# Performance work log

Measured on AMD Instinct MI355X. Metric: run time of the kernel, lower is better.

The kernel has to match this reference:

```python
import jax, jax.numpy as jnp
import numpy as np

EMBED_DIM = 256
NUM_HEADS = 8
PROJ_DIM = EMBED_DIM // NUM_HEADS


def setup_inputs() -> dict:
    key = jax.random.key(0)
    ks = jax.random.split(key, 5)
    scale = 1.0 / np.sqrt(EMBED_DIM)
    inputs = jax.random.normal(ks[0], (2, 12, 12, 12, EMBED_DIM), dtype=jnp.float32)
    Wq = jax.random.normal(ks[1], (EMBED_DIM, EMBED_DIM), dtype=jnp.float32) * scale
    Wk = jax.random.normal(ks[2], (EMBED_DIM, EMBED_DIM), dtype=jnp.float32) * scale
    Wv = jax.random.normal(ks[3], (EMBED_DIM, EMBED_DIM), dtype=jnp.float32) * scale
    Wo = jax.random.normal(ks[4], (EMBED_DIM, EMBED_DIM), dtype=jnp.float32) * scale
    z = jnp.zeros((EMBED_DIM,), dtype=jnp.float32)
    return {"inputs": inputs, "Wq": Wq, "bq": z, "Wk": Wk, "bk": z,
            "Wv": Wv, "bv": z, "Wo": Wo, "bo": z}


def reference(inputs, Wq, bq, Wk, bk, Wv, bv, Wo, bo):
    B, h, w, d, E = inputs.shape
    S = h * w * d  # flattened spatial sequence
    x = inputs.reshape(B, S, E)
    # projections + head split: [B, S, E] -> [B, H, S, P]
    def split_heads(t):
        return t.reshape(B, S, NUM_HEADS, PROJ_DIM).transpose(0, 2, 1, 3)
    q = split_heads(x @ Wq + bq)
    k = split_heads(x @ Wk + bk)
    v = split_heads(x @ Wv + bv)
    # NOTE: original module does NOT scale by 1/sqrt(proj_dim)
    scores = jnp.einsum('bhsp,bhtp->bhst', q, k)  # [B, H, S, S]
    attn = jax.nn.softmax(scores, axis=-1)
    out = jnp.einsum('bhst,bhtp->bhsp', attn, v)  # [B, H, S, P]
    out = out.transpose(0, 2, 1, 3).reshape(B, h, w, d, E)
    return out @ Wo + bo
```

## Files before the change

### kernel.cpp

```cpp
#include <hip/hip_runtime.h>
#include <math.h>

#define EMBED 256
#define HEADS 8
#define PDIM  32
#define BATCH 2
#define SEQ   1728
#define NTOK  (BATCH*SEQ)
#define NE    (NTOK*EMBED)
#define NKT   (SEQ/64)
#define LOG2E 1.44269504088896f

typedef __attribute__((ext_vector_type(8))) __bf16 bf16x8;
typedef __attribute__((ext_vector_type(4))) float  f32x4;
typedef unsigned short ushort_t;
typedef unsigned int   uint_t;

static __device__ __forceinline__ unsigned short f2bf_rne(float f) {
    union { float f; unsigned u; } x; x.f = f;
    unsigned r = x.u + 0x7fffu + ((x.u >> 16) & 1u);
    return (unsigned short)(r >> 16);
}
union v8cast { uint4 u; bf16x8 v; };

static __device__ __forceinline__ void cvt8_hilo(const float f[8], bf16x8& hi, bf16x8& lo) {
    uint4 ph, pl;
    uint_t* phv = (uint_t*)&ph; uint_t* plv = (uint_t*)&pl;
    #pragma unroll
    for (int j = 0; j < 4; ++j) {
        const float f0 = f[2 * j], f1 = f[2 * j + 1];
        const uint_t u0 = __float_as_uint(f0) + 0x8000u;
        const uint_t u1 = __float_as_uint(f1) + 0x8000u;
        phv[j] = __builtin_amdgcn_perm(u1, u0, 0x07060302u);
        const float l0 = f0 - __uint_as_float(u0 & 0xFFFF0000u);
        const float l1 = f1 - __uint_as_float(u1 & 0xFFFF0000u);
        plv[j] = __builtin_amdgcn_perm(__float_as_uint(l1) + 0x8000u,
                                       __float_as_uint(l0) + 0x8000u, 0x07060302u);
    }
    v8cast ch; ch.u = ph; hi = ch.v;
    v8cast cl; cl.u = pl; lo = cl.v;
}

__global__ __launch_bounds__(64) void qkv_gemm_kernel(
    const float* __restrict__ x,
    const float* __restrict__ Wq, const float* __restrict__ bq,
    const float* __restrict__ Wk, const float* __restrict__ bk,
    const float* __restrict__ Wv, const float* __restrict__ bv,
    ushort_t* __restrict__ qo, ushort_t* __restrict__ ko, ushort_t* __restrict__ vt)
{
    const int lane = threadIdx.x, li = lane & 15, quad = lane >> 4;
    const int m0 = blockIdx.x * 64, n0 = blockIdx.y * 32, z = blockIdx.z;
    const float* __restrict__ W    = (z == 0) ? Wq : (z == 1) ? Wk : Wv;
    const float* __restrict__ bias = (z == 0) ? bq : (z == 1) ? bk : bv;

    const float* ap = x + (size_t)(m0 + li) * EMBED + quad * 8;

    f32x4 acc[4][2];
    #pragma unroll
    for (int mt = 0; mt < 4; ++mt)
        #pragma unroll
        for (int nt = 0; nt < 2; ++nt)
            acc[mt][nt] = (f32x4){0.f, 0.f, 0.f, 0.f};

    #pragma unroll 2
    for (int k0 = 0; k0 < EMBED; k0 += 32) {
        bf16x8 ah[4], al[4];
        #pragma unroll
        for (int mt = 0; mt < 4; ++mt) {
            float af[8];
            *(float4*)&af[0] = *(const float4*)(ap + (size_t)mt * 16 * EMBED + k0);
            *(float4*)&af[4] = *(const float4*)(ap + (size_t)mt * 16 * EMBED + k0 + 4);
            cvt8_hilo(af, ah[mt], al[mt]);
        }
        bf16x8 bh[2], bl[2];
        #pragma unroll
        for (int nt = 0; nt < 2; ++nt) {
            const int n = n0 + nt * 16 + li;
            const float* wp = W + (size_t)(k0 + quad * 8) * EMBED + n;
            float bf[8];
            #pragma unroll
            for (int jj = 0; jj < 8; ++jj) bf[jj] = wp[(size_t)jj * EMBED];
            cvt8_hilo(bf, bh[nt], bl[nt]);
        }
        #pragma unroll
        for (int mt = 0; mt < 4; ++mt)
            #pragma unroll
            for (int nt = 0; nt < 2; ++nt) {
                acc[mt][nt] = __builtin_amdgcn_mfma_f32_16x16x32_bf16(ah[mt], bh[nt], acc[mt][nt], 0, 0, 0);
                acc[mt][nt] = __builtin_amdgcn_mfma_f32_16x16x32_bf16(al[mt], bh[nt], acc[mt][nt], 0, 0, 0);
                acc[mt][nt] = __builtin_amdgcn_mfma_f32_16x16x32_bf16(ah[mt], bl[nt], acc[mt][nt], 0, 0, 0);
            }
    }

    const int b = m0 / SEQ;
    const int sbase = m0 - b * SEQ;

    if (z <= 1) {
        ushort_t* __restrict__ dst = z ? ko : qo;
        #pragma unroll
        for (int nt = 0; nt < 2; ++nt) {
            const int gcol = n0 + nt * 16 + li;
            const int h = gcol >> 5, p = gcol & 31;
            const float bb = bias[gcol];
            ushort_t* base = dst + ((size_t)(b * HEADS + h) * SEQ) * PDIM + p;
            #pragma unroll
            for (int mt = 0; mt < 4; ++mt)
                #pragma unroll
                for (int r = 0; r < 4; ++r) {
                    const int s = sbase + mt * 16 + quad * 4 + r;
                    base[(size_t)s * PDIM] = f2bf_rne(acc[mt][nt][r] + bb);
                }
        }
    } else {
        #pragma unroll
        for (int nt = 0; nt < 2; ++nt) {
            const int gcol = n0 + nt * 16 + li;
            const int h = gcol >> 5, p = gcol & 31;
            const float bb = bias[gcol];
            ushort_t* base = vt + ((size_t)(b * HEADS + h) * PDIM + p) * SEQ;
            #pragma unroll
            for (int mt = 0; mt < 4; ++mt) {
                const int s0 = sbase + mt * 16 + quad * 4;
                ushort4 w;
                w.x = f2bf_rne(acc[mt][nt][0] + bb);
                w.y = f2bf_rne(acc[mt][nt][1] + bb);
                w.z = f2bf_rne(acc[mt][nt][2] + bb);
                w.w = f2bf_rne(acc[mt][nt][3] + bb);
                *(ushort4*)&base[s0] = w;
            }
        }
    }
}

__global__ __launch_bounds__(256) void attn_kernel(
    const ushort_t* __restrict__ q, const ushort_t* __restrict__ k,
    const ushort_t* __restrict__ vt, ushort_t* __restrict__ aob)
{
    const int t    = threadIdx.x;
    const int lane = t & 63;
    const int w    = t >> 6;
    const int li   = lane & 15;
    const int quad = lane >> 4;
    const int bh = blockIdx.y;
    const int b  = bh >> 3, h = bh & 7;
    const int q0 = blockIdx.x * 64 + w * 16;

    const ushort_t* __restrict__ qb = q  + (size_t)bh * SEQ * PDIM;
    const ushort_t* __restrict__ kb = k  + (size_t)bh * SEQ * PDIM;
    const ushort_t* __restrict__ vb = vt + (size_t)bh * PDIM * SEQ;

    __shared__ ushort_t Ks[2][64][40];
    __shared__ ushort_t Vs[2][32][72];
    __shared__ ushort_t Ps[4][16][72];

    const bf16x8 qfrag = *(const bf16x8*)(qb + (size_t)(q0 + li) * PDIM + quad * 8);

    const int jk = w * 16 + (lane >> 2), ck = (lane & 3) * 8;
    const int pv = w * 8 + (lane >> 3),  cv = (lane & 7) * 8;
    const ushort_t* kgp = kb + (size_t)jk * PDIM + ck;
    const ushort_t* vgp = vb + (size_t)pv * SEQ + cv;

    f32x4 o0 = {0.f, 0.f, 0.f, 0.f};
    f32x4 o1 = {0.f, 0.f, 0.f, 0.f};
    float m_run = -__builtin_inff(), l_run = 0.f;

    uint4 kreg = *(const uint4*)(kgp);
    uint4 vreg = *(const uint4*)(vgp);

    for (int kt = 0; kt < NKT; ++kt) {
        const int p = kt & 1;
        *(uint4*)&Ks[p][jk][ck] = kreg;
        *(uint4*)&Vs[p][pv][cv] = vreg;
        __syncthreads();
        if (kt + 1 < NKT) {
            kreg = *(const uint4*)(kgp + (size_t)(kt + 1) * 64 * PDIM);
            vreg = *(const uint4*)(vgp + (kt + 1) * 64);
        }

        const f32x4 zero = {0.f, 0.f, 0.f, 0.f};
        f32x4 st[4];
        #pragma unroll
        for (int jt = 0; jt < 4; ++jt) {
            const bf16x8 kf = *(const bf16x8*)&Ks[p][jt * 16 + li][quad * 8];
            st[jt] = __builtin_amdgcn_mfma_f32_16x16x32_bf16(kf, qfrag, zero, 0, 0, 0);
        }

        float tm = st[0][0];
        #pragma unroll
        for (int jt = 0; jt < 4; ++jt)
            #pragma unroll
            for (int r = 0; r < 4; ++r) tm = fmaxf(tm, st[jt][r]);
        tm = fmaxf(tm, __shfl_xor(tm, 16));
        tm = fmaxf(tm, __shfl_xor(tm, 32));
        const float mnew  = fmaxf(m_run, tm);
        const float negml = -(mnew * LOG2E);

        float ps = 0.f;
        #pragma unroll
        for (int jt = 0; jt < 4; ++jt) {
            const float p0 = __builtin_amdgcn_exp2f(fmaf(st[jt][0], LOG2E, negml));
            const float p1 = __builtin_amdgcn_exp2f(fmaf(st[jt][1], LOG2E, negml));
            const float p2 = __builtin_amdgcn_exp2f(fmaf(st[jt][2], LOG2E, negml));
            const float p3 = __builtin_amdgcn_exp2f(fmaf(st[jt][3], LOG2E, negml));
            ps += (p0 + p1) + (p2 + p3);
            uint2 pw;
            pw.x = __builtin_amdgcn_perm(__float_as_uint(p1) + 0x8000u,
                                         __float_as_uint(p0) + 0x8000u, 0x07060302u);
            pw.y = __builtin_amdgcn_perm(__float_as_uint(p3) + 0x8000u,
                                         __float_as_uint(p2) + 0x8000u, 0x07060302u);
            *(uint2*)&Ps[w][li][16 * jt + 4 * quad] = pw;
        }
        ps += __shfl_xor(ps, 16);
        ps += __shfl_xor(ps, 32);

        const float alpha = __builtin_amdgcn_exp2f(fmaf(m_run, LOG2E, negml));
        l_run = fmaf(l_run, alpha, ps);
        m_run = mnew;

        float af[4];
        #pragma unroll
        for (int r = 0; r < 4; ++r) af[r] = __shfl(alpha, 4 * quad + r);
        #pragma unroll
        for (int r = 0; r < 4; ++r) { o0[r] *= af[r]; o1[r] *= af[r]; }

        const bf16x8 pa0 = *(const bf16x8*)&Ps[w][li][8 * quad];
        const bf16x8 pa1 = *(const bf16x8*)&Ps[w][li][32 + 8 * quad];
        const bf16x8 vf00 = *(const bf16x8*)&Vs[p][li][quad * 8];
        const bf16x8 vf01 = *(const bf16x8*)&Vs[p][16 + li][quad * 8];
        const bf16x8 vf10 = *(const bf16x8*)&Vs[p][li][32 + quad * 8];
        const bf16x8 vf11 = *(const bf16x8*)&Vs[p][16 + li][32 + quad * 8];
        o0 = __builtin_amdgcn_mfma_f32_16x16x32_bf16(pa0, vf00, o0, 0, 0, 0);
        o0 = __builtin_amdgcn_mfma_f32_16x16x32_bf16(pa1, vf10, o0, 0, 0, 0);
        o1 = __builtin_amdgcn_mfma_f32_16x16x32_bf16(pa0, vf01, o1, 0, 0, 0);
        o1 = __builtin_amdgcn_mfma_f32_16x16x32_bf16(pa1, vf11, o1, 0, 0, 0);
    }

    float linv[4];
    #pragma unroll
    for (int r = 0; r < 4; ++r) linv[r] = 1.0f / __shfl(l_run, 4 * quad + r);
    #pragma unroll
    for (int r = 0; r < 4; ++r) {
        const int s = q0 + 4 * quad + r;
        ushort_t* row = aob + ((size_t)(b * SEQ + s)) * EMBED + h * PDIM;
        row[li]      = f2bf_rne(o0[r] * linv[r]);
        row[16 + li] = f2bf_rne(o1[r] * linv[r]);
    }
}

__global__ __launch_bounds__(64) void out_gemm_kernel(
    const ushort_t* __restrict__ a, const float* __restrict__ Wo,
    const float* __restrict__ bo, float* __restrict__ out)
{
    const int lane = threadIdx.x, li = lane & 15, quad = lane >> 4;
    const int m0 = blockIdx.x * 64, n0 = blockIdx.y * 16;

    const ushort_t* aph = a + (size_t)(m0 + li) * EMBED + quad * 8;

    f32x4 acc[4];
    #pragma unroll
    for (int mt = 0; mt < 4; ++mt) acc[mt] = (f32x4){0.f, 0.f, 0.f, 0.f};

    #pragma unroll 2
    for (int k0 = 0; k0 < EMBED; k0 += 32) {
        bf16x8 ah[4];
        #pragma unroll
        for (int mt = 0; mt < 4; ++mt)
            ah[mt] = *(const bf16x8*)(aph + (size_t)mt * 16 * EMBED + k0);
        const float* wp = Wo + (size_t)(k0 + quad * 8) * EMBED + n0 + li;
        uint4 pb;
        uint_t* pbv = (uint_t*)&pb;
        #pragma unroll
        for (int j = 0; j < 4; ++j) {
            const uint_t u0 = __float_as_uint(wp[(size_t)(2 * j) * EMBED])     + 0x8000u;
            const uint_t u1 = __float_as_uint(wp[(size_t)(2 * j + 1) * EMBED]) + 0x8000u;
            pbv[j] = __builtin_amdgcn_perm(u1, u0, 0x07060302u);
        }
        v8cast cb; cb.u = pb;
        #pragma unroll
        for (int mt = 0; mt < 4; ++mt)
            acc[mt] = __builtin_amdgcn_mfma_f32_16x16x32_bf16(ah[mt], cb.v, acc[mt], 0, 0, 0);
    }

    const float bb = bo[n0 + li];
    #pragma unroll
    for (int mt = 0; mt < 4; ++mt)
        #pragma unroll
        for (int r = 0; r < 4; ++r) {
            const int row = m0 + mt * 16 + quad * 4 + r;
            out[(size_t)row * EMBED + n0 + li] = acc[mt][r] + bb;
        }
}

extern "C" void kernel_launch(void* const* d_in, const int* in_sizes, int n_in,
                              void* d_out, int out_size, void* d_ws, size_t ws_size,
                              hipStream_t stream)
{
    const float* x  = (const float*)d_in[0];
    const float* Wq = (const float*)d_in[1];
    const float* bq = (const float*)d_in[2];
    const float* Wk = (const float*)d_in[3];
    const float* bk = (const float*)d_in[4];
    const float* Wv = (const float*)d_in[5];
    const float* bv = (const float*)d_in[6];
    const float* Wo = (const float*)d_in[7];
    const float* bo = (const float*)d_in[8];
    float* out = (float*)d_out;

    ushort_t* ws  = (ushort_t*)d_ws;
    ushort_t* qb  = ws;
    ushort_t* kb  = qb + (size_t)NE;
    ushort_t* vt  = kb + (size_t)NE;
    ushort_t* aob = vt + (size_t)NE;

    qkv_gemm_kernel<<<dim3(NTOK / 64, 8, 3), 64, 0, stream>>>(
        x, Wq, bq, Wk, bk, Wv, bv, qb, kb, vt);
    attn_kernel<<<dim3(SEQ / 64, BATCH * HEADS), 256, 0, stream>>>(qb, kb, vt, aob);
    out_gemm_kernel<<<dim3(NTOK / 64, 16), 64, 0, stream>>>(aob, Wo, bo, out);
}
```

Before: 121.5 us.

## Fuse QKV, attention and out-projection into one cooperative persistent kernel

Replaces three separate launches with one cooperative kernel of 432 blocks that runs the QKV GEMM tiles, then a grid sync, then attention, then another grid sync, then the output projection. The goal is to remove per-launch overhead and the idle tails between dependent stages. The output projection also uses smaller 32-row tiles so its work spreads over the persistent blocks. In exchange it pays for two grid-wide barriers, is limited to a fixed grid with 2 blocks per CU, and falls back to the old three-kernel path if the cooperative launch is not possible.

```diff
diff --git a/kernel.cpp b/kernel.cpp
--- a/kernel.cpp
+++ b/kernel.cpp
@@ -1,4 +1,5 @@
 #include <hip/hip_runtime.h>
+#include <hip/hip_cooperative_groups.h>
 #include <math.h>
 
 #define EMBED 256
@@ -10,6 +11,8 @@
 #define NE    (NTOK*EMBED)
 #define NKT   (SEQ/64)
 #define LOG2E 1.44269504088896f
+#define NBLK  432
+#define NTHR  256
 
 typedef __attribute__((ext_vector_type(8))) __bf16 bf16x8;
 typedef __attribute__((ext_vector_type(4))) float  f32x4;
@@ -41,6 +44,278 @@
     v8cast cl; cl.u = pl; lo = cl.v;
 }
 
+
+static __device__ __forceinline__ void qkv_tile(
+    int wg, int li, int quad,
+    const float* __restrict__ x,
+    const float* __restrict__ Wq, const float* __restrict__ bq,
+    const float* __restrict__ Wk, const float* __restrict__ bk,
+    const float* __restrict__ Wv, const float* __restrict__ bv,
+    ushort_t* __restrict__ qg, ushort_t* __restrict__ kg, ushort_t* __restrict__ vg)
+{
+    const int z   = wg / 432;
+    const int rem = wg - z * 432;
+    const int my  = rem % 54, ny = rem / 54;
+    const int m0  = my * 64, n0 = ny * 32;
+    const float* __restrict__ W    = (z == 0) ? Wq : (z == 1) ? Wk : Wv;
+    const float* __restrict__ bias = (z == 0) ? bq : (z == 1) ? bk : bv;
+
+    const float* ap = x + (size_t)(m0 + li) * EMBED + quad * 8;
+
+    f32x4 acc[4][2];
+    #pragma unroll
+    for (int mt = 0; mt < 4; ++mt)
+        #pragma unroll
+        for (int nt = 0; nt < 2; ++nt)
+            acc[mt][nt] = (f32x4){0.f, 0.f, 0.f, 0.f};
+
+    #pragma unroll 2
+    for (int k0 = 0; k0 < EMBED; k0 += 32) {
+        bf16x8 ah[4], al[4];
+        #pragma unroll
+        for (int mt = 0; mt < 4; ++mt) {
+            float af[8];
+            *(float4*)&af[0] = *(const float4*)(ap + (size_t)mt * 16 * EMBED + k0);
+            *(float4*)&af[4] = *(const float4*)(ap + (size_t)mt * 16 * EMBED + k0 + 4);
+            cvt8_hilo(af, ah[mt], al[mt]);
+        }
+        bf16x8 bh[2], bl[2];
+        #pragma unroll
+        for (int nt = 0; nt < 2; ++nt) {
+            const int n = n0 + nt * 16 + li;
+            const float* wp = W + (size_t)(k0 + quad * 8) * EMBED + n;
+            float bf[8];
+            #pragma unroll
+            for (int jj = 0; jj < 8; ++jj) bf[jj] = wp[(size_t)jj * EMBED];
+            cvt8_hilo(bf, bh[nt], bl[nt]);
+        }
+        #pragma unroll
+        for (int mt = 0; mt < 4; ++mt)
+            #pragma unroll
+            for (int nt = 0; nt < 2; ++nt) {
+                acc[mt][nt] = __builtin_amdgcn_mfma_f32_16x16x32_bf16(ah[mt], bh[nt], acc[mt][nt], 0, 0, 0);
+                acc[mt][nt] = __builtin_amdgcn_mfma_f32_16x16x32_bf16(al[mt], bh[nt], acc[mt][nt], 0, 0, 0);
+                acc[mt][nt] = __builtin_amdgcn_mfma_f32_16x16x32_bf16(ah[mt], bl[nt], acc[mt][nt], 0, 0, 0);
+            }
+    }
+
+    const int b = m0 / SEQ;
+    const int sbase = m0 - b * SEQ;
+
+    if (z <= 1) {
+        ushort_t* __restrict__ dst = z ? kg : qg;
+        #pragma unroll
+        for (int nt = 0; nt < 2; ++nt) {
+            const int gcol = n0 + nt * 16 + li;
+            const int h = gcol >> 5, p = gcol & 31;
+            const float bb = bias[gcol];
+            ushort_t* base = dst + ((size_t)(b * HEADS + h) * SEQ) * PDIM + p;
+            #pragma unroll
+            for (int mt = 0; mt < 4; ++mt)
+                #pragma unroll
+                for (int r = 0; r < 4; ++r) {
+                    const int s = sbase + mt * 16 + quad * 4 + r;
+                    base[(size_t)s * PDIM] = f2bf_rne(acc[mt][nt][r] + bb);
+                }
+        }
+    } else {
+        #pragma unroll
+        for (int nt = 0; nt < 2; ++nt) {
+            const int gcol = n0 + nt * 16 + li;
+            const int h = gcol >> 5, p = gcol & 31;
+            const float bb = bias[gcol];
+            ushort_t* base = vg + ((size_t)(b * HEADS + h) * PDIM + p) * SEQ;
+            #pragma unroll
+            for (int mt = 0; mt < 4; ++mt) {
+                const int s0 = sbase + mt * 16 + quad * 4;
+                ushort4 wv4;
+                wv4.x = f2bf_rne(acc[mt][nt][0] + bb);
+                wv4.y = f2bf_rne(acc[mt][nt][1] + bb);
+                wv4.z = f2bf_rne(acc[mt][nt][2] + bb);
+                wv4.w = f2bf_rne(acc[mt][nt][3] + bb);
+                *(ushort4*)&base[s0] = wv4;
+            }
+        }
+    }
+}
+
+static __device__ __forceinline__ void outproj_tile(
+    int wg, int li, int quad,
+    const ushort_t* __restrict__ ag, const float* __restrict__ Wo,
+    const float* __restrict__ bo, float* __restrict__ out)
+{
+    const int my = wg % 108, ny = wg / 108;
+    const int m0 = my * 32, n0 = ny * 16;
+
+    const ushort_t* aph = ag + (size_t)(m0 + li) * EMBED + quad * 8;
+
+    f32x4 acc[2];
+    acc[0] = (f32x4){0.f, 0.f, 0.f, 0.f};
+    acc[1] = (f32x4){0.f, 0.f, 0.f, 0.f};
+
+    #pragma unroll 2
+    for (int k0 = 0; k0 < EMBED; k0 += 32) {
+        const bf16x8 a0 = *(const bf16x8*)(aph + k0);
+        const bf16x8 a1 = *(const bf16x8*)(aph + 16 * EMBED + k0);
+        const float* wp = Wo + (size_t)(k0 + quad * 8) * EMBED + n0 + li;
+        uint4 pb;
+        uint_t* pbv = (uint_t*)&pb;
+        #pragma unroll
+        for (int j = 0; j < 4; ++j) {
+            const uint_t u0 = __float_as_uint(wp[(size_t)(2 * j) * EMBED])     + 0x8000u;
+            const uint_t u1 = __float_as_uint(wp[(size_t)(2 * j + 1) * EMBED]) + 0x8000u;
+            pbv[j] = __builtin_amdgcn_perm(u1, u0, 0x07060302u);
+        }
+        v8cast cb; cb.u = pb;
+        acc[0] = __builtin_amdgcn_mfma_f32_16x16x32_bf16(a0, cb.v, acc[0], 0, 0, 0);
+        acc[1] = __builtin_amdgcn_mfma_f32_16x16x32_bf16(a1, cb.v, acc[1], 0, 0, 0);
+    }
+
+    const float bb = bo[n0 + li];
+    #pragma unroll
+    for (int mt = 0; mt < 2; ++mt)
+        #pragma unroll
+        for (int r = 0; r < 4; ++r) {
+            const int row = m0 + mt * 16 + quad * 4 + r;
+            out[(size_t)row * EMBED + n0 + li] = acc[mt][r] + bb;
+        }
+}
+
+__global__ __launch_bounds__(256, 2) void fused_mhsa_kernel(
+    const float* __restrict__ x,
+    const float* __restrict__ Wq, const float* __restrict__ bq,
+    const float* __restrict__ Wk, const float* __restrict__ bk,
+    const float* __restrict__ Wv, const float* __restrict__ bv,
+    const float* __restrict__ Wo, const float* __restrict__ bo,
+    float* __restrict__ out,
+    ushort_t* __restrict__ qg, ushort_t* __restrict__ kg,
+    ushort_t* __restrict__ vg, ushort_t* __restrict__ ag)
+{
+    const int t    = threadIdx.x;
+    const int lane = t & 63, w = t >> 6;
+    const int li   = lane & 15, quad = lane >> 4;
+    const int bid  = blockIdx.x;
+
+    {
+        const int wg = bid * 4 + w;
+        if (wg < 1296)
+            qkv_tile(wg, li, quad, x, Wq, bq, Wk, bk, Wv, bv, qg, kg, vg);
+    }
+
+    cooperative_groups::this_grid().sync();
+
+    {
+        const int bh = bid & 15, qt = bid >> 4;
+        const int b  = bh >> 3, h = bh & 7;
+        const int q0 = qt * 64 + w * 16;
+
+        const ushort_t* __restrict__ qb = qg + (size_t)bh * SEQ * PDIM;
+        const ushort_t* __restrict__ kb = kg + (size_t)bh * SEQ * PDIM;
+        const ushort_t* __restrict__ vb = vg + (size_t)bh * PDIM * SEQ;
+
+        __shared__ ushort_t Ks[2][64][40];
+        __shared__ ushort_t Vs[2][32][72];
+        __shared__ ushort_t Ps[4][16][72];
+
+        const bf16x8 qfrag = *(const bf16x8*)(qb + (size_t)(q0 + li) * PDIM + quad * 8);
+
+        const int jk = w * 16 + (lane >> 2), ck = (lane & 3) * 8;
+        const int pv = w * 8 + (lane >> 3),  cv = (lane & 7) * 8;
+        const ushort_t* kgp = kb + (size_t)jk * PDIM + ck;
+        const ushort_t* vgp = vb + (size_t)pv * SEQ + cv;
+
+        f32x4 o0 = {0.f, 0.f, 0.f, 0.f};
+        f32x4 o1 = {0.f, 0.f, 0.f, 0.f};
+        float m_run = -__builtin_inff(), l_run = 0.f;
+
+        uint4 kreg = *(const uint4*)(kgp);
+        uint4 vreg = *(const uint4*)(vgp);
+
+        for (int kt = 0; kt < NKT; ++kt) {
+            const int p = kt & 1;
+            *(uint4*)&Ks[p][jk][ck] = kreg;
+            *(uint4*)&Vs[p][pv][cv] = vreg;
+            __syncthreads();
+            if (kt + 1 < NKT) {
+                kreg = *(const uint4*)(kgp + (size_t)(kt + 1) * 64 * PDIM);
+                vreg = *(const uint4*)(vgp + (kt + 1) * 64);
+            }
+
+            const f32x4 zero = {0.f, 0.f, 0.f, 0.f};
+            f32x4 st[4];
+            #pragma unroll
+            for (int jt = 0; jt < 4; ++jt) {
+                const bf16x8 kf = *(const bf16x8*)&Ks[p][jt * 16 + li][quad * 8];
+                st[jt] = __builtin_amdgcn_mfma_f32_16x16x32_bf16(kf, qfrag, zero, 0, 0, 0);
+            }
+
+            float tm = st[0][0];
+            #pragma unroll
+            for (int jt = 0; jt < 4; ++jt)
+                #pragma unroll
+                for (int r = 0; r < 4; ++r) tm = fmaxf(tm, st[jt][r]);
+            tm = fmaxf(tm, __shfl_xor(tm, 16));
+            tm = fmaxf(tm, __shfl_xor(tm, 32));
+            const float mnew  = fmaxf(m_run, tm);
+            const float negml = -(mnew * LOG2E);
+
+            float ps = 0.f;
+            #pragma unroll
+            for (int jt = 0; jt < 4; ++jt) {
+                const float p0 = __builtin_amdgcn_exp2f(fmaf(st[jt][0], LOG2E, negml));
+                const float p1 = __builtin_amdgcn_exp2f(fmaf(st[jt][1], LOG2E, negml));
+                const float p2 = __builtin_amdgcn_exp2f(fmaf(st[jt][2], LOG2E, negml));
+                const float p3 = __builtin_amdgcn_exp2f(fmaf(st[jt][3], LOG2E, negml));
+                ps += (p0 + p1) + (p2 + p3);
+                uint2 pw;
+                pw.x = __builtin_amdgcn_perm(__float_as_uint(p1) + 0x8000u,
+                                             __float_as_uint(p0) + 0x8000u, 0x07060302u);
+                pw.y = __builtin_amdgcn_perm(__float_as_uint(p3) + 0x8000u,
+                                             __float_as_uint(p2) + 0x8000u, 0x07060302u);
+                *(uint2*)&Ps[w][li][16 * jt + 4 * quad] = pw;
+            }
+            ps += __shfl_xor(ps, 16);
+            ps += __shfl_xor(ps, 32);
+
+            const float alpha = __builtin_amdgcn_exp2f(fmaf(m_run, LOG2E, negml));
+            l_run = fmaf(l_run, alpha, ps);
+            m_run = mnew;
+
+            float af[4];
+            #pragma unroll
+            for (int r = 0; r < 4; ++r) af[r] = __shfl(alpha, 4 * quad + r);
+            #pragma unroll
+            for (int r = 0; r < 4; ++r) { o0[r] *= af[r]; o1[r] *= af[r]; }
+
+            const bf16x8 pa0 = *(const bf16x8*)&Ps[w][li][8 * quad];
+            const bf16x8 pa1 = *(const bf16x8*)&Ps[w][li][32 + 8 * quad];
+            const bf16x8 vf00 = *(const bf16x8*)&Vs[p][li][quad * 8];
+            const bf16x8 vf01 = *(const bf16x8*)&Vs[p][16 + li][quad * 8];
+            const bf16x8 vf10 = *(const bf16x8*)&Vs[p][li][32 + quad * 8];
+            const bf16x8 vf11 = *(const bf16x8*)&Vs[p][16 + li][32 + quad * 8];
+            o0 = __builtin_amdgcn_mfma_f32_16x16x32_bf16(pa0, vf00, o0, 0, 0, 0);
+            o0 = __builtin_amdgcn_mfma_f32_16x16x32_bf16(pa1, vf10, o0, 0, 0, 0);
+            o1 = __builtin_amdgcn_mfma_f32_16x16x32_bf16(pa0, vf01, o1, 0, 0, 0);
+            o1 = __builtin_amdgcn_mfma_f32_16x16x32_bf16(pa1, vf11, o1, 0, 0, 0);
+        }
+
+        float linv[4];
+        #pragma unroll
+        for (int r = 0; r < 4; ++r) linv[r] = 1.0f / __shfl(l_run, 4 * quad + r);
+        #pragma unroll
+        for (int r = 0; r < 4; ++r) {
+            const int s = q0 + 4 * quad + r;
+            ushort_t* row = ag + ((size_t)(b * SEQ + s)) * EMBED + h * PDIM;
+            row[li]      = f2bf_rne(o0[r] * linv[r]);
+            row[16 + li] = f2bf_rne(o1[r] * linv[r]);
+        }
+    }
+
+    cooperative_groups::this_grid().sync();
+
+    outproj_tile(bid * 4 + w, li, quad, ag, Wo, bo, out);
+}
+
 __global__ __launch_bounds__(64) void qkv_gemm_kernel(
     const float* __restrict__ x,
     const float* __restrict__ Wq, const float* __restrict__ bq,
@@ -49,87 +324,10 @@
     ushort_t* __restrict__ qo, ushort_t* __restrict__ ko, ushort_t* __restrict__ vt)
 {
     const int lane = threadIdx.x, li = lane & 15, quad = lane >> 4;
-    const int m0 = blockIdx.x * 64, n0 = blockIdx.y * 32, z = blockIdx.z;
-    const float* __restrict__ W    = (z == 0) ? Wq : (z == 1) ? Wk : Wv;
-    const float* __restrict__ bias = (z == 0) ? bq : (z == 1) ? bk : bv;
-
-    const float* ap = x + (size_t)(m0 + li) * EMBED + quad * 8;
-
-    f32x4 acc[4][2];
-    #pragma unroll
-    for (int mt = 0; mt < 4; ++mt)
-        #pragma unroll
-        for (int nt = 0; nt < 2; ++nt)
-            acc[mt][nt] = (f32x4){0.f, 0.f, 0.f, 0.f};
-
-    #pragma unroll 2
-    for (int k0 = 0; k0 < EMBED; k0 += 32) {
-        bf16x8 ah[4], al[4];
-        #pragma unroll
-        for (int mt = 0; mt < 4; ++mt) {
-            float af[8];
-            *(float4*)&af[0] = *(const float4*)(ap + (size_t)mt * 16 * EMBED + k0);
-            *(float4*)&af[4] = *(const float4*)(ap + (size_t)mt * 16 * EMBED + k0 + 4);
-            cvt8_hilo(af, ah[mt], al[mt]);
-        }
-        bf16x8 bh[2], bl[2];
-        #pragma unroll
-        for (int nt = 0; nt < 2; ++nt) {
-            const int n = n0 + nt * 16 + li;
-            const float* wp = W + (size_t)(k0 + quad * 8) * EMBED + n;
-            float bf[8];
-            #pragma unroll
-            for (int jj = 0; jj < 8; ++jj) bf[jj] = wp[(size_t)jj * EMBED];
-            cvt8_hilo(bf, bh[nt], bl[nt]);
-        }
-        #pragma unroll
-        for (int mt = 0; mt < 4; ++mt)
-            #pragma unroll
-            for (int nt = 0; nt < 2; ++nt) {
-                acc[mt][nt] = __builtin_amdgcn_mfma_f32_16x16x32_bf16(ah[mt], bh[nt], acc[mt][nt], 0, 0, 0);
-                acc[mt][nt] = __builtin_amdgcn_mfma_f32_16x16x32_bf16(al[mt], bh[nt], acc[mt][nt], 0, 0, 0);
-                acc[mt][nt] = __builtin_amdgcn_mfma_f32_16x16x32_bf16(ah[mt], bl[nt], acc[mt][nt], 0, 0, 0);
-            }
-    }
-
-    const int b = m0 / SEQ;
-    const int sbase = m0 - b * SEQ;
-
-    if (z <= 1) {
-        ushort_t* __restrict__ dst = z ? ko : qo;
-        #pragma unroll
-        for (int nt = 0; nt < 2; ++nt) {
-            const int gcol = n0 + nt * 16 + li;
-            const int h = gcol >> 5, p = gcol & 31;
-            const float bb = bias[gcol];
-            ushort_t* base = dst + ((size_t)(b * HEADS + h) * SEQ) * PDIM + p;
-            #pragma unroll
-            for (int mt = 0; mt < 4; ++mt)
-                #pragma unroll
-                for (int r = 0; r < 4; ++r) {
-                    const int s = sbase + mt * 16 + quad * 4 + r;
-                    base[(size_t)s * PDIM] = f2bf_rne(acc[mt][nt][r] + bb);
-                }
-        }
-    } else {
-        #pragma unroll
-        for (int nt = 0; nt < 2; ++nt) {
-            const int gcol = n0 + nt * 16 + li;
-            const int h = gcol >> 5, p = gcol & 31;
-            const float bb = bias[gcol];
-            ushort_t* base = vt + ((size_t)(b * HEADS + h) * PDIM + p) * SEQ;
-            #pragma unroll
-            for (int mt = 0; mt < 4; ++mt) {
-                const int s0 = sbase + mt * 16 + quad * 4;
-                ushort4 w;
-                w.x = f2bf_rne(acc[mt][nt][0] + bb);
-                w.y = f2bf_rne(acc[mt][nt][1] + bb);
-                w.z = f2bf_rne(acc[mt][nt][2] + bb);
-                w.w = f2bf_rne(acc[mt][nt][3] + bb);
-                *(ushort4*)&base[s0] = w;
-            }
-        }
-    }
+    const int wg = (blockIdx.z * 8 + blockIdx.y) * 54 + blockIdx.x;
+    qkv_tile(blockIdx.z * 432 + blockIdx.y * 54 + blockIdx.x, li, quad,
+             x, Wq, bq, Wk, bk, Wv, bv, qo, ko, vt);
+    (void)wg;
 }
 
 __global__ __launch_bounds__(256) void attn_kernel(
@@ -137,10 +335,8 @@
     const ushort_t* __restrict__ vt, ushort_t* __restrict__ aob)
 {
     const int t    = threadIdx.x;
-    const int lane = t & 63;
-    const int w    = t >> 6;
-    const int li   = lane & 15;
-    const int quad = lane >> 4;
+    const int lane = t & 63, w = t >> 6;
+    const int li   = lane & 15, quad = lane >> 4;
     const int bh = blockIdx.y;
     const int b  = bh >> 3, h = bh & 7;
     const int q0 = blockIdx.x * 64 + w * 16;
@@ -252,43 +448,7 @@
     const float* __restrict__ bo, float* __restrict__ out)
 {
     const int lane = threadIdx.x, li = lane & 15, quad = lane >> 4;
-    const int m0 = blockIdx.x * 64, n0 = blockIdx.y * 16;
-
-    const ushort_t* aph = a + (size_t)(m0 + li) * EMBED + quad * 8;
-
-    f32x4 acc[4];
-    #pragma unroll
-    for (int mt = 0; mt < 4; ++mt) acc[mt] = (f32x4){0.f, 0.f, 0.f, 0.f};
-
-    #pragma unroll 2
-    for (int k0 = 0; k0 < EMBED; k0 += 32) {
-        bf16x8 ah[4];
-        #pragma unroll
-        for (int mt = 0; mt < 4; ++mt)
-            ah[mt] = *(const bf16x8*)(aph + (size_t)mt * 16 * EMBED + k0);
-        const float* wp = Wo + (size_t)(k0 + quad * 8) * EMBED + n0 + li;
-        uint4 pb;
-        uint_t* pbv = (uint_t*)&pb;
-        #pragma unroll
-        for (int j = 0; j < 4; ++j) {
-            const uint_t u0 = __float_as_uint(wp[(size_t)(2 * j) * EMBED])     + 0x8000u;
-            const uint_t u1 = __float_as_uint(wp[(size_t)(2 * j + 1) * EMBED]) + 0x8000u;
-            pbv[j] = __builtin_amdgcn_perm(u1, u0, 0x07060302u);
-        }
-        v8cast cb; cb.u = pb;
-        #pragma unroll
-        for (int mt = 0; mt < 4; ++mt)
-            acc[mt] = __builtin_amdgcn_mfma_f32_16x16x32_bf16(ah[mt], cb.v, acc[mt], 0, 0, 0);
-    }
-
-    const float bb = bo[n0 + li];
-    #pragma unroll
-    for (int mt = 0; mt < 4; ++mt)
-        #pragma unroll
-        for (int r = 0; r < 4; ++r) {
-            const int row = m0 + mt * 16 + quad * 4 + r;
-            out[(size_t)row * EMBED + n0 + li] = acc[mt][r] + bb;
-        }
+    outproj_tile(blockIdx.y * 108 + blockIdx.x, li, quad, a, Wo, bo, out);
 }
 
 extern "C" void kernel_launch(void* const* d_in, const int* in_sizes, int n_in,
@@ -306,14 +466,28 @@
     const float* bo = (const float*)d_in[8];
     float* out = (float*)d_out;
 
-    ushort_t* ws  = (ushort_t*)d_ws;
-    ushort_t* qb  = ws;
-    ushort_t* kb  = qb + (size_t)NE;
-    ushort_t* vt  = kb + (size_t)NE;
-    ushort_t* aob = vt + (size_t)NE;
-
-    qkv_gemm_kernel<<<dim3(NTOK / 64, 8, 3), 64, 0, stream>>>(
-        x, Wq, bq, Wk, bk, Wv, bv, qb, kb, vt);
-    attn_kernel<<<dim3(SEQ / 64, BATCH * HEADS), 256, 0, stream>>>(qb, kb, vt, aob);
-    out_gemm_kernel<<<dim3(NTOK / 64, 16), 64, 0, stream>>>(aob, Wo, bo, out);
-}
+    ushort_t* ws = (ushort_t*)d_ws;
+    ushort_t* qg = ws;
+    ushort_t* kg = qg + (size_t)NE;
+    ushort_t* vg = kg + (size_t)NE;
+    ushort_t* ag = vg + (size_t)NE;
+
+    int maxb = 0;
+    hipError_t qerr = hipOccupancyMaxActiveBlocksPerMultiprocessor(
+        &maxb, (const void*)fused_mhsa_kernel, NTHR, 0);
+    bool coop_done = false;
+    if (qerr == hipSuccess && maxb >= 2) {
+        void* args[] = { (void*)&x, (void*)&Wq, (void*)&bq, (void*)&Wk, (void*)&bk,
+                         (void*)&Wv, (void*)&bv, (void*)&Wo, (void*)&bo, (void*)&out,
+                         (void*)&qg, (void*)&kg, (void*)&vg, (void*)&ag };
+        hipError_t lerr = hipLaunchCooperativeKernel((const void*)fused_mhsa_kernel,
+                                                     dim3(NBLK), dim3(NTHR), args, 0, stream);
+        coop_done = (lerr == hipSuccess);
+    }
+    if (!coop_done) {
+        qkv_gemm_kernel<<<dim3(54, 8, 3), 64, 0, stream>>>(
+            x, Wq, bq, Wk, bk, Wv, bv, qg, kg, vg);
+        attn_kernel<<<dim3(SEQ / 64, BATCH * HEADS), 256, 0, stream>>>(qg, kg, vg, ag);
+        out_gemm_kernel<<<dim3(108, 16), 64, 0, stream>>>(ag, Wo, bo, out);
+    }
+}
```

Result: slower. 237.5 us (+95.5%).

## Split attention KV range across wave pairs and merge partial softmax results

Applied to the files above, without the earlier changes.

The attention kernel now handles 32 queries per block instead of 64. Each pair of waves splits the 27 key tiles into two halves (tiles 0–13 and 13–26, with the second half skipping its first tile). Partial outputs and running max/sum are combined through shared memory at the end. This doubles the grid to 864 blocks to improve occupancy and latency hiding across CUs. The cost is a shared-memory merge step and extra synchronisation, and each thread loads two vectors per tile.

```diff
diff --git a/kernel.cpp b/kernel.cpp
--- a/kernel.cpp
+++ b/kernel.cpp
@@ -8,7 +8,6 @@
 #define SEQ   1728
 #define NTOK  (BATCH*SEQ)
 #define NE    (NTOK*EMBED)
-#define NKT   (SEQ/64)
 #define LOG2E 1.44269504088896f
 
 typedef __attribute__((ext_vector_type(8))) __bf16 bf16x8;
@@ -121,12 +120,12 @@
             #pragma unroll
             for (int mt = 0; mt < 4; ++mt) {
                 const int s0 = sbase + mt * 16 + quad * 4;
-                ushort4 w;
-                w.x = f2bf_rne(acc[mt][nt][0] + bb);
-                w.y = f2bf_rne(acc[mt][nt][1] + bb);
-                w.z = f2bf_rne(acc[mt][nt][2] + bb);
-                w.w = f2bf_rne(acc[mt][nt][3] + bb);
-                *(ushort4*)&base[s0] = w;
+                ushort4 wv4;
+                wv4.x = f2bf_rne(acc[mt][nt][0] + bb);
+                wv4.y = f2bf_rne(acc[mt][nt][1] + bb);
+                wv4.z = f2bf_rne(acc[mt][nt][2] + bb);
+                wv4.w = f2bf_rne(acc[mt][nt][3] + bb);
+                *(ushort4*)&base[s0] = wv4;
             }
         }
     }
@@ -137,13 +136,13 @@
     const ushort_t* __restrict__ vt, ushort_t* __restrict__ aob)
 {
     const int t    = threadIdx.x;
-    const int lane = t & 63;
-    const int w    = t >> 6;
-    const int li   = lane & 15;
-    const int quad = lane >> 4;
+    const int lane = t & 63, w = t >> 6;
+    const int li   = lane & 15, quad = lane >> 4;
+    const int pr   = w >> 1;
+    const int c    = w & 1;
     const int bh = blockIdx.y;
     const int b  = bh >> 3, h = bh & 7;
-    const int q0 = blockIdx.x * 64 + w * 16;
+    const int q0 = blockIdx.x * 32 + pr * 16;
 
     const ushort_t* __restrict__ qb = q  + (size_t)bh * SEQ * PDIM;
     const ushort_t* __restrict__ kb = k  + (size_t)bh * SEQ * PDIM;
@@ -152,11 +151,13 @@
     __shared__ ushort_t Ks[2][64][40];
     __shared__ ushort_t Vs[2][32][72];
     __shared__ ushort_t Ps[4][16][72];
+    __shared__ float OS[2][16][32];
+    __shared__ float mS[2][16], lS[2][16];
 
     const bf16x8 qfrag = *(const bf16x8*)(qb + (size_t)(q0 + li) * PDIM + quad * 8);
 
-    const int jk = w * 16 + (lane >> 2), ck = (lane & 3) * 8;
-    const int pv = w * 8 + (lane >> 3),  cv = (lane & 7) * 8;
+    const int jk = pr * 32 + (lane >> 1), ck = (lane & 1) * 8;
+    const int pv = pr * 16 + (lane >> 2), cv = (lane & 3) * 8;
     const ushort_t* kgp = kb + (size_t)jk * PDIM + ck;
     const ushort_t* vgp = vb + (size_t)pv * SEQ + cv;
 
@@ -164,86 +165,117 @@
     f32x4 o1 = {0.f, 0.f, 0.f, 0.f};
     float m_run = -__builtin_inff(), l_run = 0.f;
 
-    uint4 kreg = *(const uint4*)(kgp);
-    uint4 vreg = *(const uint4*)(vgp);
-
-    for (int kt = 0; kt < NKT; ++kt) {
-        const int p = kt & 1;
-        *(uint4*)&Ks[p][jk][ck] = kreg;
-        *(uint4*)&Vs[p][pv][cv] = vreg;
+    const int kt0 = c ? 13 : 0;
+
+    uint4 kr0 = *(const uint4*)(kgp + (size_t)kt0 * 64 * PDIM);
+    uint4 kr1 = *(const uint4*)(kgp + (size_t)kt0 * 64 * PDIM + 16);
+    uint4 vr0 = *(const uint4*)(vgp + kt0 * 64);
+    uint4 vr1 = *(const uint4*)(vgp + kt0 * 64 + 32);
+
+    for (int it = 0; it < 14; ++it) {
         __syncthreads();
-        if (kt + 1 < NKT) {
-            kreg = *(const uint4*)(kgp + (size_t)(kt + 1) * 64 * PDIM);
-            vreg = *(const uint4*)(vgp + (kt + 1) * 64);
-        }
-
-        const f32x4 zero = {0.f, 0.f, 0.f, 0.f};
-        f32x4 st[4];
-        #pragma unroll
-        for (int jt = 0; jt < 4; ++jt) {
-            const bf16x8 kf = *(const bf16x8*)&Ks[p][jt * 16 + li][quad * 8];
-            st[jt] = __builtin_amdgcn_mfma_f32_16x16x32_bf16(kf, qfrag, zero, 0, 0, 0);
-        }
-
-        float tm = st[0][0];
-        #pragma unroll
-        for (int jt = 0; jt < 4; ++jt)
-            #pragma unroll
-            for (int r = 0; r < 4; ++r) tm = fmaxf(tm, st[jt][r]);
-        tm = fmaxf(tm, __shfl_xor(tm, 16));
-        tm = fmaxf(tm, __shfl_xor(tm, 32));
-        const float mnew  = fmaxf(m_run, tm);
-        const float negml = -(mnew * LOG2E);
-
-        float ps = 0.f;
-        #pragma unroll
-        for (int jt = 0; jt < 4; ++jt) {
-            const float p0 = __builtin_amdgcn_exp2f(fmaf(st[jt][0], LOG2E, negml));
-            const float p1 = __builtin_amdgcn_exp2f(fmaf(st[jt][1], LOG2E, negml));
-            const float p2 = __builtin_amdgcn_exp2f(fmaf(st[jt][2], LOG2E, negml));
-            const float p3 = __builtin_amdgcn_exp2f(fmaf(st[jt][3], LOG2E, negml));
-            ps += (p0 + p1) + (p2 + p3);
-            uint2 pw;
-            pw.x = __builtin_amdgcn_perm(__float_as_uint(p1) + 0x8000u,
-                                         __float_as_uint(p0) + 0x8000u, 0x07060302u);
-            pw.y = __builtin_amdgcn_perm(__float_as_uint(p3) + 0x8000u,
-                                         __float_as_uint(p2) + 0x8000u, 0x07060302u);
-            *(uint2*)&Ps[w][li][16 * jt + 4 * quad] = pw;
-        }
-        ps += __shfl_xor(ps, 16);
-        ps += __shfl_xor(ps, 32);
-
-        const float alpha = __builtin_amdgcn_exp2f(fmaf(m_run, LOG2E, negml));
-        l_run = fmaf(l_run, alpha, ps);
-        m_run = mnew;
-
-        float af[4];
-        #pragma unroll
-        for (int r = 0; r < 4; ++r) af[r] = __shfl(alpha, 4 * quad + r);
-        #pragma unroll
-        for (int r = 0; r < 4; ++r) { o0[r] *= af[r]; o1[r] *= af[r]; }
-
-        const bf16x8 pa0 = *(const bf16x8*)&Ps[w][li][8 * quad];
-        const bf16x8 pa1 = *(const bf16x8*)&Ps[w][li][32 + 8 * quad];
-        const bf16x8 vf00 = *(const bf16x8*)&Vs[p][li][quad * 8];
-        const bf16x8 vf01 = *(const bf16x8*)&Vs[p][16 + li][quad * 8];
-        const bf16x8 vf10 = *(const bf16x8*)&Vs[p][li][32 + quad * 8];
-        const bf16x8 vf11 = *(const bf16x8*)&Vs[p][16 + li][32 + quad * 8];
-        o0 = __builtin_amdgcn_mfma_f32_16x16x32_bf16(pa0, vf00, o0, 0, 0, 0);
-        o0 = __builtin_amdgcn_mfma_f32_16x16x32_bf16(pa1, vf10, o0, 0, 0, 0);
-        o1 = __builtin_amdgcn_mfma_f32_16x16x32_bf16(pa0, vf01, o1, 0, 0, 0);
-        o1 = __builtin_amdgcn_mfma_f32_16x16x32_bf16(pa1, vf11, o1, 0, 0, 0);
-    }
-
-    float linv[4];
-    #pragma unroll
-    for (int r = 0; r < 4; ++r) linv[r] = 1.0f / __shfl(l_run, 4 * quad + r);
-    #pragma unroll
-    for (int r = 0; r < 4; ++r) {
-        const int s = q0 + 4 * quad + r;
-        ushort_t* row = aob + ((size_t)(b * SEQ + s)) * EMBED + h * PDIM;
-        row[li]      = f2bf_rne(o0[r] * linv[r]);
-        row[16 + li] = f2bf_rne(o1[r] * linv[r]);
+        *(uint4*)&Ks[c][jk][ck]      = kr0;
+        *(uint4*)&Ks[c][jk][ck + 16] = kr1;
+        *(uint4*)&Vs[c][pv][cv]      = vr0;
+        *(uint4*)&Vs[c][pv][cv + 32] = vr1;
+        __syncthreads();
+        if (it + 1 < 14) {
+            const int tn = kt0 + it + 1;
+            kr0 = *(const uint4*)(kgp + (size_t)tn * 64 * PDIM);
+            kr1 = *(const uint4*)(kgp + (size_t)tn * 64 * PDIM + 16);
+            vr0 = *(const uint4*)(vgp + tn * 64);
+            vr1 = *(const uint4*)(vgp + tn * 64 + 32);
+        }
+
+        if (c == 0 || it > 0) {
+            const f32x4 zero = {0.f, 0.f, 0.f, 0.f};
+            f32x4 st[4];
+            #pragma unroll
+            for (int jt = 0; jt < 4; ++jt) {
+                const bf16x8 kf = *(const bf16x8*)&Ks[c][jt * 16 + li][quad * 8];
+                st[jt] = __builtin_amdgcn_mfma_f32_16x16x32_bf16(kf, qfrag, zero, 0, 0, 0);
+            }
+
+            float tm = st[0][0];
+            #pragma unroll
+            for (int jt = 0; jt < 4; ++jt)
+                #pragma unroll
+                for (int r = 0; r < 4; ++r) tm = fmaxf(tm, st[jt][r]);
+            tm = fmaxf(tm, __shfl_xor(tm, 16));
+            tm = fmaxf(tm, __shfl_xor(tm, 32));
+            const float mnew  = fmaxf(m_run, tm);
+            const float negml = -(mnew * LOG2E);
+
+            float ps = 0.f;
+            #pragma unroll
+            for (int jt = 0; jt < 4; ++jt) {
+                const float p0 = __builtin_amdgcn_exp2f(fmaf(st[jt][0], LOG2E, negml));
+                const float p1 = __builtin_amdgcn_exp2f(fmaf(st[jt][1], LOG2E, negml));
+                const float p2 = __builtin_amdgcn_exp2f(fmaf(st[jt][2], LOG2E, negml));
+                const float p3 = __builtin_amdgcn_exp2f(fmaf(st[jt][3], LOG2E, negml));
+                ps += (p0 + p1) + (p2 + p3);
+                uint2 pw;
+                pw.x = __builtin_amdgcn_perm(__float_as_uint(p1) + 0x8000u,
+                                             __float_as_uint(p0) + 0x8000u, 0x07060302u);
+                pw.y = __builtin_amdgcn_perm(__float_as_uint(p3) + 0x8000u,
+                                             __float_as_uint(p2) + 0x8000u, 0x07060302u);
+                *(uint2*)&Ps[w][li][16 * jt + 4 * quad] = pw;
+            }
+            ps += __shfl_xor(ps, 16);
+            ps += __shfl_xor(ps, 32);
+
+            const float alpha = __builtin_amdgcn_exp2f(fmaf(m_run, LOG2E, negml));
+            l_run = fmaf(l_run, alpha, ps);
+            m_run = mnew;
+
+            float af[4];
+            #pragma unroll
+            for (int r = 0; r < 4; ++r) af[r] = __shfl(alpha, 4 * quad + r);
+            #pragma unroll
+            for (int r = 0; r < 4; ++r) { o0[r] *= af[r]; o1[r] *= af[r]; }
+
+            const bf16x8 pa0 = *(const bf16x8*)&Ps[w][li][8 * quad];
+            const bf16x8 pa1 = *(const bf16x8*)&Ps[w][li][32 + 8 * quad];
+            const bf16x8 vf00 = *(const bf16x8*)&Vs[c][li][quad * 8];
+            const bf16x8 vf01 = *(const bf16x8*)&Vs[c][16 + li][quad * 8];
+            const bf16x8 vf10 = *(const bf16x8*)&Vs[c][li][32 + quad * 8];
+            const bf16x8 vf11 = *(const bf16x8*)&Vs[c][16 + li][32 + quad * 8];
+            o0 = __builtin_amdgcn_mfma_f32_16x16x32_bf16(pa0, vf00, o0, 0, 0, 0);
+            o0 = __builtin_amdgcn_mfma_f32_16x16x32_bf16(pa1, vf10, o0, 0, 0, 0);
+            o1 = __builtin_amdgcn_mfma_f32_16x16x32_bf16(pa0, vf01, o1, 0, 0, 0);
+            o1 = __builtin_amdgcn_mfma_f32_16x16x32_bf16(pa1, vf11, o1, 0, 0, 0);
+        }
+    }
+
+    __syncthreads();
+    if (c == 1) {
+        if (quad == 0) { mS[pr][li] = m_run; lS[pr][li] = l_run; }
+        #pragma unroll
+        for (int r = 0; r < 4; ++r) {
+            OS[pr][4 * quad + r][li]      = o0[r];
+            OS[pr][4 * quad + r][16 + li] = o1[r];
+        }
+    }
+    __syncthreads();
+    if (c == 0) {
+        const float m1 = mS[pr][li], l1 = lS[pr][li];
+        const float M  = fmaxf(m_run, m1);
+        const float a0 = __builtin_amdgcn_exp2f((m_run - M) * LOG2E);
+        const float a1 = __builtin_amdgcn_exp2f((m1    - M) * LOG2E);
+        const float lt = a0 * l_run + a1 * l1;
+        #pragma unroll
+        for (int r = 0; r < 4; ++r) {
+            const int row = 4 * quad + r;
+            const float af0  = __shfl(a0, row);
+            const float af1  = __shfl(a1, row);
+            const float linv = 1.0f / __shfl(lt, row);
+            const float v0 = (af0 * o0[r] + af1 * OS[pr][row][li])      * linv;
+            const float v1 = (af0 * o1[r] + af1 * OS[pr][row][16 + li]) * linv;
+            const int s = q0 + row;
+            ushort_t* orow = aob + ((size_t)(b * SEQ + s)) * EMBED + h * PDIM;
+            orow[li]      = f2bf_rne(v0);
+            orow[16 + li] = f2bf_rne(v1);
+        }
     }
 }
 
@@ -306,14 +338,14 @@
     const float* bo = (const float*)d_in[8];
     float* out = (float*)d_out;
 
-    ushort_t* ws  = (ushort_t*)d_ws;
-    ushort_t* qb  = ws;
-    ushort_t* kb  = qb + (size_t)NE;
-    ushort_t* vt  = kb + (size_t)NE;
-    ushort_t* aob = vt + (size_t)NE;
-
-    qkv_gemm_kernel<<<dim3(NTOK / 64, 8, 3), 64, 0, stream>>>(
-        x, Wq, bq, Wk, bk, Wv, bv, qb, kb, vt);
-    attn_kernel<<<dim3(SEQ / 64, BATCH * HEADS), 256, 0, stream>>>(qb, kb, vt, aob);
-    out_gemm_kernel<<<dim3(NTOK / 64, 16), 64, 0, stream>>>(aob, Wo, bo, out);
-}
+    ushort_t* ws = (ushort_t*)d_ws;
+    ushort_t* qg = ws;
+    ushort_t* kg = qg + (size_t)NE;
+    ushort_t* vg = kg + (size_t)NE;
+    ushort_t* ag = vg + (size_t)NE;
+
+    qkv_gemm_kernel<<<dim3(54, 8, 3), 64, 0, stream>>>(
+        x, Wq, bq, Wk, bk, Wv, bv, qg, kg, vg);
+    attn_kernel<<<dim3(54, 16), 256, 0, stream>>>(qg, kg, vg, ag);
+    out_gemm_kernel<<<dim3(54, 16), 64, 0, stream>>>(ag, Wo, bo, out);
+}
```

Measured after the change: 121.7 us. Within noise of the previous version (+0.1%).
